# Optimization experiments

Measured on AMD Instinct MI355X. Metric: run time of the kernel, lower is better.

## Reference

```python
import jax, jax.numpy as jnp
import numpy as np

N, F_IN, H, C, E = 50000, 512, 128, 64, 800000


def setup_inputs() -> dict:
    key = jax.random.key(0)
    ks = jax.random.split(key, 20)
    stdv = 1.0 / np.sqrt(H)
    std_att = 1.0
    std_att_vec = 1.0 / np.sqrt(3.0)
    u = lambda k, shape, s: jax.random.uniform(k, shape, jnp.float32, -s, s)
    inp = {
        "x": jax.random.normal(ks[0], (N, F_IN), jnp.float32),
        "edge_row": jax.random.randint(ks[1], (E,), 0, N, jnp.int32),
        "edge_col": jax.random.randint(ks[2], (E,), 0, N, jnp.int32),
        "edge_val": jax.random.uniform(ks[3], (E,), jnp.float32) * (1.0 / 16.0),
        "weight_low": u(ks[4], (F_IN, H), stdv),
        "weight_high": u(ks[5], (F_IN, H), stdv),
        "weight_mlp": u(ks[6], (F_IN, H), stdv),
        "att_vec_low": u(ks[7], (H, 1), std_att),
        "att_vec_high": u(ks[8], (H, 1), std_att),
        "att_vec_mlp": u(ks[9], (H, 1), std_att),
        "att_vec": u(ks[10], (3, 3), std_att_vec),
        "weight_low2": u(ks[11], (H, C), stdv),
        "weight_high2": u(ks[12], (H, C), stdv),
        "weight_mlp2": u(ks[13], (H, C), stdv),
        "att_vec_low2": u(ks[14], (C, 1), std_att),
        "att_vec_high2": u(ks[15], (C, 1), std_att),
        "att_vec_mlp2": u(ks[16], (C, 1), std_att),
        "att_vec2": u(ks[17], (3, 3), std_att_vec),
    }
    return inp


def _spmm_low(row, col, val, X):
    # adj_low @ X via gather + segment-sum over edges
    return jax.ops.segment_sum(val[:, None] * X[col], row, num_segments=N)


def _attention(o_low, o_high, o_mlp, a_low, a_high, a_mlp, a_vec):
    T = 3.0
    feats = jnp.concatenate([o_low @ a_low, o_high @ a_high, o_mlp @ a_mlp], axis=1)  # [N,3]
    att = jax.nn.softmax(jax.nn.sigmoid(feats) @ a_vec / T, axis=1)
    return att[:, 0:1], att[:, 1:2], att[:, 2:3]


def _layer(X, row, col, val, W_l, W_h, W_m, a_l, a_h, a_m, a_vec):
    xl = X @ W_l
    xh = X @ W_h
    o_low = jax.nn.relu(_spmm_low(row, col, val, xl))
    o_high = jax.nn.relu(xh - _spmm_low(row, col, val, xh))  # (I - adj_low) @ xh
    o_mlp = jax.nn.relu(X @ W_m)
    al, ah, am = _attention(o_low, o_high, o_mlp, a_l, a_h, a_m, a_vec)
    return 3.0 * (al * o_low + ah * o_high + am * o_mlp)


def reference(x, edge_row, edge_col, edge_val, weight_low, weight_high, weight_mlp,
              att_vec_low, att_vec_high, att_vec_mlp, att_vec,
              weight_low2, weight_high2, weight_mlp2,
              att_vec_low2, att_vec_high2, att_vec_mlp2, att_vec2):
    h = _layer(x, edge_row, edge_col, edge_val, weight_low, weight_high, weight_mlp,
               att_vec_low, att_vec_high, att_vec_mlp, att_vec)
    out = _layer(h, edge_row, edge_col, edge_val, weight_low2, weight_high2, weight_mlp2,
                 att_vec_low2, att_vec_high2, att_vec_mlp2, att_vec2)
    return jax.nn.log_softmax(out, axis=1)
```

## Files before the change

kernel.cpp:

```cpp
#include <hip/hip_runtime.h>
#include <hip/hip_bf16.h>

#define NN 50000
#define F_IN 512
#define HH 128
#define CC 64

typedef __attribute__((ext_vector_type(8))) short short8v;
typedef __attribute__((ext_vector_type(4))) float f32x4;
typedef __attribute__((ext_vector_type(2))) float f32x2;

__device__ __forceinline__ short f2b(float f) {
    unsigned u = __builtin_bit_cast(unsigned, f);
    unsigned r = (u + 0x7fffu + ((u >> 16) & 1u)) >> 16;
    return (short)r;
}
__device__ __forceinline__ float b2f(short s) {
    unsigned u = ((unsigned)(unsigned short)s) << 16;
    return __builtin_bit_cast(float, u);
}
__device__ __forceinline__ float b2f_lo(unsigned p) {
    return __builtin_bit_cast(float, p << 16);
}
__device__ __forceinline__ float b2f_hi(unsigned p) {
    return __builtin_bit_cast(float, p & 0xffff0000u);
}

__device__ __forceinline__ f32x2 q2_lo(unsigned p) {
    return __builtin_amdgcn_cvt_pk_f32_fp8(p, false);
}
__device__ __forceinline__ f32x2 q2_hi(unsigned p) {
    return __builtin_amdgcn_cvt_pk_f32_fp8(p, true);
}

__device__ __forceinline__ int xcd_swz(int bid, int nwg) {
    int q = nwg >> 3, r = nwg & 7;
    int xcd = bid & 7, off = bid >> 3;
    return (xcd < r ? xcd * (q + 1) : r * (q + 1) + (xcd - r) * q) + off;
}

__device__ __forceinline__ void load_lds16(const short* g, short* l) {
    __builtin_amdgcn_global_load_lds(
        (const __attribute__((address_space(1))) unsigned int*)g,
        (__attribute__((address_space(3))) unsigned int*)l,
        16, 0, 0);
}

template <int K, int OUTW>
__device__ __forceinline__ void wprep_body(const float* __restrict__ W0,
                                           const float* __restrict__ W1,
                                           const float* __restrict__ W2,
                                           short* __restrict__ Bt, int id) {
    const int nth = 3 * OUTW * (K / 8);
    if (id >= nth) return;
    const int n = id / (K / 8);
    const int kq = id % (K / 8);
    const int sel = n / OUTW;
    const int c = n % OUTW;
    const float* W = sel == 0 ? W0 : (sel == 1 ? W1 : W2);
    short v[8];
#pragma unroll
    for (int j = 0; j < 8; ++j) v[j] = f2b(W[(size_t)(kq * 8 + j) * OUTW + c]);
#pragma unroll
    for (int j = 0; j < 8; ++j) Bt[(size_t)n * K + kq * 8 + j] = v[j];
}

__global__ __launch_bounds__(256) void prep0(int* __restrict__ counts, int n,
                                             const float* __restrict__ Wl,
                                             const float* __restrict__ Wh,
                                             const float* __restrict__ Wm,
                                             short* __restrict__ Bt1,
                                             const float* __restrict__ Wl2,
                                             const float* __restrict__ Wh2,
                                             const float* __restrict__ Wm2,
                                             short* __restrict__ Bt2,
                                             int nZero, int nW1) {
    const int b = blockIdx.x;
    if (b < nZero) {
        int i = b * 256 + threadIdx.x;
        if (i < n) counts[i] = 0;
    } else if (b < nZero + nW1) {
        wprep_body<F_IN, HH>(Wl, Wh, Wm, Bt1, (b - nZero) * 256 + threadIdx.x);
    } else {
        wprep_body<HH, CC>(Wl2, Wh2, Wm2, Bt2, (b - nZero - nW1) * 256 + threadIdx.x);
    }
}

__global__ __launch_bounds__(256) void hist_xconv(const int* __restrict__ erow,
                                                  int* __restrict__ counts, int E,
                                                  const float* __restrict__ x,
                                                  short* __restrict__ xb, int n8,
                                                  int nHist) {
    const int b = blockIdx.x;
    const int total = gridDim.x;
    const long hb4 = ((long)b * nHist) / total;
    const long ha4 = ((long)(b + 1) * nHist) / total;
    if (ha4 != hb4) {
        int i = (int)hb4 * 256 + threadIdx.x;
        if (i < E) atomicAdd(&counts[erow[i]], 1);
        return;
    }
    int i = (b - (int)hb4) * 256 + threadIdx.x;
    if (i >= n8) return;
    const float4* xp = (const float4*)x;
    const float4 a = xp[2 * i];
    const float4 bb = xp[2 * i + 1];
    short8v o;
    o[0] = f2b(a.x); o[1] = f2b(a.y); o[2] = f2b(a.z); o[3] = f2b(a.w);
    o[4] = f2b(bb.x); o[5] = f2b(bb.y); o[6] = f2b(bb.z); o[7] = f2b(bb.w);
    *reinterpret_cast<short8v*>(&xb[(size_t)i * 8]) = o;
}

template <int K, int BNout>
__device__ __forceinline__ void gemm_body(const short* __restrict__ A,
                                          const short* __restrict__ Bt,
                                          short* __restrict__ xl,
                                          short* __restrict__ xh,
                                          short* __restrict__ xm,
                                          int M, int wg, short* smem) {
    constexpr int BM = 128, BK = 64;
    constexpr int FM = (BNout == 128) ? 4 : 2;
    constexpr int FN = 4;
    constexpr int WM = FM * 16;
    constexpr int NKT = K / BK;
    constexpr int NBL = BNout / 32;

    short* As = smem;
    short* Bs = smem + BM * BK;

    const int tid = threadIdx.x;
    const int lane = tid & 63;
    const int wid = tid >> 6;
    const int bm = wg / 3;
    const int bn = wg % 3;
    const int m0 = bm * BM;
    const int n0 = bn * BNout;
    const int wm = (BNout == 128) ? (wid >> 1) : wid;
    const int wn = (BNout == 128) ? (wid & 1) : 0;

    const int r8 = lane >> 3;
    const int sl = (lane & 7) ^ r8;

    f32x4 acc[FM][FN];
#pragma unroll
    for (int i = 0; i < FM; ++i)
#pragma unroll
        for (int j = 0; j < FN; ++j) acc[i][j] = (f32x4){0.f, 0.f, 0.f, 0.f};

    for (int kt = 0; kt < NKT; ++kt) {
        const int k0 = kt * BK;
        __syncthreads();
#pragma unroll
        for (int i = 0; i < 4; ++i) {
            int r = (wid * 4 + i) * 8 + r8;
            int gr = m0 + r; if (gr >= M) gr = M - 1;
            load_lds16(&A[(size_t)gr * K + k0 + sl * 8], &As[(wid * 4 + i) * 512]);
        }
#pragma unroll
        for (int i = 0; i < NBL; ++i) {
            int r = (wid * NBL + i) * 8 + r8;
            load_lds16(&Bt[(size_t)(n0 + r) * K + k0 + sl * 8],
                       &Bs[(wid * NBL + i) * 512]);
        }
        __syncthreads();

        const int mrow = lane & 15;
        const int kg = lane >> 4;
#pragma unroll
        for (int kk = 0; kk < 2; ++kk) {
            short8v af[FM], bf[FN];
#pragma unroll
            for (int f = 0; f < FM; ++f) {
                int m = wm * WM + f * 16 + mrow;
                int s = kk * 4 + kg;
                af[f] = *reinterpret_cast<const short8v*>(
                    &As[m * 64 + ((s ^ (m & 7)) << 3)]);
            }
#pragma unroll
            for (int f = 0; f < FN; ++f) {
                int nr = wn * 64 + f * 16 + mrow;
                int s = kk * 4 + kg;
                bf[f] = *reinterpret_cast<const short8v*>(
                    &Bs[nr * 64 + ((s ^ (nr & 7)) << 3)]);
            }
#pragma unroll
            for (int i = 0; i < FM; ++i)
#pragma unroll
                for (int j = 0; j < FN; ++j)
                    acc[i][j] = __builtin_amdgcn_mfma_f32_16x16x32_bf16(
                        af[i], bf[j], acc[i][j], 0, 0, 0);
        }
    }

    __syncthreads();
#pragma unroll
    for (int i = 0; i < FM; ++i)
#pragma unroll
        for (int j = 0; j < FN; ++j) {
            int cc = wn * 64 + j * 16 + (lane & 15);
#pragma unroll
            for (int e = 0; e < 4; ++e) {
                int r = wm * WM + i * 16 + (lane >> 4) * 4 + e;
                smem[r * BNout + cc] = f2b(acc[i][j][e]);
            }
        }
    __syncthreads();

    short* plane = (bn == 0) ? xl : ((bn == 1) ? xh : xm);
    constexpr int CH = BM * BNout / 8;
#pragma unroll
    for (int p = 0; p < CH / 256; ++p) {
        int idx = p * 256 + tid;
        int r = idx / (BNout / 8);
        int c8 = idx % (BNout / 8);
        int grow = m0 + r;
        if (grow < M)
            *reinterpret_cast<int4*>(&plane[(size_t)grow * BNout + c8 * 8]) =
                *reinterpret_cast<const int4*>(&smem[r * BNout + c8 * 8]);
    }
}

template <int K, int BNout>
__global__ __launch_bounds__(256) void gemm_scatter(const short* __restrict__ A,
                                                    const short* __restrict__ Bt,
                                                    short* __restrict__ xl,
                                                    short* __restrict__ xh,
                                                    short* __restrict__ xm,
                                                    int M, int nGemm,
                                                    const int* __restrict__ row,
                                                    const int* __restrict__ col,
                                                    const float* __restrict__ val,
                                                    int* __restrict__ cursor,
                                                    int2* __restrict__ edges, int E,
                                                    int nScat) {
    __shared__ short smem[128 * 64 + BNout * 64];

    const int total = nGemm + nScat;
    const int swz = xcd_swz(blockIdx.x, total);
    const long ns_b = ((long)swz * nScat) / total;
    const long ns_a = ((long)(swz + 1) * nScat) / total;

    if (ns_a != ns_b) {
        int i = (int)ns_b * 256 + threadIdx.x;
        if (i < E) {
            int r = row[i];
            int p = atomicAdd(&cursor[r], 1);
            int2 rec;
            rec.x = col[i];
            rec.y = __builtin_bit_cast(int, val[i]);
            edges[p] = rec;
        }
        return;
    }
    gemm_body<K, BNout>(A, Bt, xl, xh, xm, M, swz - (int)ns_b, smem);
}

template <int K, int BNout>
__global__ __launch_bounds__(256) void gemm_mfma(const short* __restrict__ A,
                                                 const short* __restrict__ Bt,
                                                 short* __restrict__ xl,
                                                 short* __restrict__ xh,
                                                 short* __restrict__ xm,
                                                 int M) {
    __shared__ short smem[128 * 64 + BNout * 64];
    gemm_body<K, BNout>(A, Bt, xl, xh, xm, M, xcd_swz(blockIdx.x, gridDim.x), smem);
}

__global__ __launch_bounds__(256) void pack8_1(const unsigned* __restrict__ xl,
                                               const unsigned* __restrict__ xh,
                                               unsigned* __restrict__ xq, int n) {
    int i = blockIdx.x * 256 + threadIdx.x;
    if (i >= n) return;
    const unsigned vx = xl[i];
    const unsigned vh = xh[i];
    unsigned r = __builtin_amdgcn_cvt_pk_fp8_f32(b2f_lo(vx), b2f_hi(vx), 0, false);
    r = __builtin_amdgcn_cvt_pk_fp8_f32(b2f_lo(vh), b2f_hi(vh), r, true);
    xq[i] = r;
}

__global__ __launch_bounds__(256) void pack8_2(const unsigned* __restrict__ xl,
                                               const unsigned* __restrict__ xh,
                                               unsigned* __restrict__ xq, int n) {
    int i = blockIdx.x * 256 + threadIdx.x;
    if (i >= n) return;
    const unsigned vx = xl[i];
    const unsigned vh = xh[i];
    unsigned r = __builtin_amdgcn_cvt_pk_fp8_f32(b2f_lo(vx), b2f_lo(vh), 0, false);
    r = __builtin_amdgcn_cvt_pk_fp8_f32(b2f_hi(vx), b2f_hi(vh), r, true);
    xq[i] = r;
}

__global__ __launch_bounds__(256) void block_sums_kernel(const int* __restrict__ counts,
                                                         int* __restrict__ bsums, int n) {
    __shared__ int s[256];
    int tid = threadIdx.x;
    int i = blockIdx.x * 256 + tid;
    s[tid] = (i < n) ? counts[i] : 0;
    __syncthreads();
#pragma unroll
    for (int off = 128; off > 0; off >>= 1) {
        if (tid < off) s[tid] += s[tid + off];
        __syncthreads();
    }
    if (tid == 0) bsums[blockIdx.x] = s[0];
}

__global__ __launch_bounds__(256) void scan_bsums_kernel(int* __restrict__ bsums, int nb) {
    __shared__ int s[256];
    int t = threadIdx.x;
    int v = (t < nb) ? bsums[t] : 0;
    s[t] = v;
    __syncthreads();
#pragma unroll
    for (int off = 1; off < 256; off <<= 1) {
        int u = (t >= off) ? s[t - off] : 0;
        __syncthreads();
        s[t] += u;
        __syncthreads();
    }
    if (t < nb) bsums[t] = s[t] - v;
}

__global__ __launch_bounds__(256) void scan_final_kernel(const int* __restrict__ counts,
                                                         const int* __restrict__ bsums,
                                                         int* __restrict__ rowptr,
                                                         int* __restrict__ cursor, int n) {
    __shared__ int s[256];
    int tid = threadIdx.x;
    int i = blockIdx.x * 256 + tid;
    int v = (i < n) ? counts[i] : 0;
    s[tid] = v;
    __syncthreads();
#pragma unroll
    for (int off = 1; off < 256; off <<= 1) {
        int t = (tid >= off) ? s[tid - off] : 0;
        __syncthreads();
        s[tid] += t;
        __syncthreads();
    }
    int excl = s[tid] - v + bsums[blockIdx.x];
    if (i < n) {
        rowptr[i] = excl;
        cursor[i] = excl;
        if (i == n - 1) rowptr[n] = excl + v;
    }
}

__device__ __forceinline__ float wave_sum(float v) {
#pragma unroll
    for (int off = 32; off > 0; off >>= 1) v += __shfl_xor(v, off, 64);
    return v;
}
__device__ __forceinline__ float wave_max(float v) {
#pragma unroll
    for (int off = 32; off > 0; off >>= 1) v = fmaxf(v, __shfl_xor(v, off, 64));
    return v;
}

__global__ __launch_bounds__(256) void spmm_att1(const int* __restrict__ rowptr,
                                                 const int2* __restrict__ edges,
                                                 const unsigned* __restrict__ xq,
                                                 const unsigned* __restrict__ xhp,
                                                 const unsigned* __restrict__ xmp,
                                                 const float* __restrict__ a_low,
                                                 const float* __restrict__ a_high,
                                                 const float* __restrict__ a_mlp,
                                                 const float* __restrict__ av,
                                                 short* __restrict__ hb,
                                                 int n) {
    const int node = blockIdx.x * 4 + (threadIdx.x >> 6);
    const int lane = threadIdx.x & 63;
    if (node >= n) return;

    const int s = __builtin_amdgcn_readfirstlane(rowptr[node]);
    const int e = __builtin_amdgcn_readfirstlane(rowptr[node + 1]);

    float l0 = 0.f, l1 = 0.f, h0 = 0.f, h1 = 0.f;
    for (int j = s; j < e; j += 8) {
        int   cq[8];
        float vq[8];
#pragma unroll
        for (int q = 0; q < 8; ++q) {
            const int jj = min(j + q, e - 1);
            const int2 rec = edges[jj];
            cq[q] = __builtin_amdgcn_readfirstlane(rec.x);
            int vb = __builtin_amdgcn_readfirstlane(rec.y);
            float t = __builtin_bit_cast(float, vb);
            vq[q] = (j + q < e) ? t : 0.f;
        }
        unsigned p[8];
#pragma unroll
        for (int q = 0; q < 8; ++q)
            p[q] = xq[(size_t)cq[q] * 64 + lane];
#pragma unroll
        for (int q = 0; q < 8; ++q) {
            const f32x2 lo = q2_lo(p[q]);
            const f32x2 hi = q2_hi(p[q]);
            l0 += vq[q] * lo.x; l1 += vq[q] * lo.y;
            h0 += vq[q] * hi.x; h1 += vq[q] * hi.y;
        }
    }

    const unsigned xhn = xhp[(size_t)node * 64 + lane];
    const unsigned xmn = xmp[(size_t)node * 64 + lane];
    float ol0 = fmaxf(l0, 0.f);
    float ol1 = fmaxf(l1, 0.f);
    float oh0 = fmaxf(b2f_lo(xhn) - h0, 0.f);
    float oh1 = fmaxf(b2f_hi(xhn) - h1, 0.f);
    float om0 = fmaxf(b2f_lo(xmn), 0.f);
    float om1 = fmaxf(b2f_hi(xmn), 0.f);

    const float2 aL = ((const float2*)a_low)[lane];
    const float2 aH = ((const float2*)a_high)[lane];
    const float2 aM = ((const float2*)a_mlp)[lane];
    float dl = wave_sum(ol0 * aL.x + ol1 * aL.y);
    float dh = wave_sum(oh0 * aH.x + oh1 * aH.y);
    float dm = wave_sum(om0 * aM.x + om1 * aM.y);

    const float g0 = 1.f / (1.f + expf(-dl));
    const float g1 = 1.f / (1.f + expf(-dh));
    const float g2 = 1.f / (1.f + expf(-dm));
    float s0 = (g0 * av[0] + g1 * av[3] + g2 * av[6]) * (1.f / 3.f);
    float s1 = (g0 * av[1] + g1 * av[4] + g2 * av[7]) * (1.f / 3.f);
    float s2 = (g0 * av[2] + g1 * av[5] + g2 * av[8]) * (1.f / 3.f);
    float mx = fmaxf(s0, fmaxf(s1, s2));
    float e0 = expf(s0 - mx), e1 = expf(s1 - mx), e2 = expf(s2 - mx);
    float inv = 1.f / (e0 + e1 + e2);
    float at0 = e0 * inv, at1 = e1 * inv, at2 = e2 * inv;

    float ho0 = 3.f * (at0 * ol0 + at1 * oh0 + at2 * om0);
    float ho1 = 3.f * (at0 * ol1 + at1 * oh1 + at2 * om1);
    unsigned pk = (unsigned)(unsigned short)f2b(ho0) |
                  ((unsigned)(unsigned short)f2b(ho1) << 16);
    ((unsigned*)hb)[(size_t)node * 64 + lane] = pk;
}

__global__ __launch_bounds__(256) void spmm_att2(const int* __restrict__ rowptr,
                                                 const int2* __restrict__ edges,
                                                 const unsigned short* __restrict__ xq,
                                                 const short* __restrict__ xhp,
                                                 const short* __restrict__ xmp,
                                                 const float* __restrict__ a_low,
                                                 const float* __restrict__ a_high,
                                                 const float* __restrict__ a_mlp,
                                                 const float* __restrict__ av,
                                                 float* __restrict__ out,
                                                 int n) {
    const int node = blockIdx.x * 4 + (threadIdx.x >> 6);
    const int lane = threadIdx.x & 63;
    if (node >= n) return;

    const int s = __builtin_amdgcn_readfirstlane(rowptr[node]);
    const int e = __builtin_amdgcn_readfirstlane(rowptr[node + 1]);

    float accl = 0.f, acch = 0.f;
    for (int j = s; j < e; j += 8) {
        int   cq[8];
        float vq[8];
#pragma unroll
        for (int q = 0; q < 8; ++q) {
            const int jj = min(j + q, e - 1);
            const int2 rec = edges[jj];
            cq[q] = __builtin_amdgcn_readfirstlane(rec.x);
            int vb = __builtin_amdgcn_readfirstlane(rec.y);
            float t = __builtin_bit_cast(float, vb);
            vq[q] = (j + q < e) ? t : 0.f;
        }
        unsigned short p[8];
#pragma unroll
        for (int q = 0; q < 8; ++q)
            p[q] = xq[(size_t)cq[q] * 64 + lane];
#pragma unroll
        for (int q = 0; q < 8; ++q) {
            const f32x2 d = q2_lo((unsigned)p[q]);
            accl += vq[q] * d.x;
            acch += vq[q] * d.y;
        }
    }

    float ol = fmaxf(accl, 0.f);
    float oh = fmaxf(b2f(xhp[(size_t)node * 64 + lane]) - acch, 0.f);
    float om = fmaxf(b2f(xmp[(size_t)node * 64 + lane]), 0.f);

    float dl = wave_sum(ol * a_low[lane]);
    float dh = wave_sum(oh * a_high[lane]);
    float dm = wave_sum(om * a_mlp[lane]);

    const float g0 = 1.f / (1.f + expf(-dl));
    const float g1 = 1.f / (1.f + expf(-dh));
    const float g2 = 1.f / (1.f + expf(-dm));
    float s0 = (g0 * av[0] + g1 * av[3] + g2 * av[6]) * (1.f / 3.f);
    float s1 = (g0 * av[1] + g1 * av[4] + g2 * av[7]) * (1.f / 3.f);
    float s2 = (g0 * av[2] + g1 * av[5] + g2 * av[8]) * (1.f / 3.f);
    float mx3 = fmaxf(s0, fmaxf(s1, s2));
    float e0 = expf(s0 - mx3), e1 = expf(s1 - mx3), e2 = expf(s2 - mx3);
    float inv = 1.f / (e0 + e1 + e2);
    float at0 = e0 * inv, at1 = e1 * inv, at2 = e2 * inv;

    float o = 3.f * (at0 * ol + at1 * oh + at2 * om);

    float m = wave_max(o);
    float ex = expf(o - m);
    float su = wave_sum(ex);
    out[(size_t)node * 64 + lane] = o - m - logf(su);
}

extern "C" void kernel_launch(void* const* d_in, const int* in_sizes, int n_in,
                              void* d_out, int out_size, void* d_ws, size_t ws_size,
                              hipStream_t stream) {
    const float* x    = (const float*)d_in[0];
    const int*   erow = (const int*)d_in[1];
    const int*   ecol = (const int*)d_in[2];
    const float* eval = (const float*)d_in[3];
    const float* Wl   = (const float*)d_in[4];
    const float* Wh   = (const float*)d_in[5];
    const float* Wm   = (const float*)d_in[6];
    const float* al   = (const float*)d_in[7];
    const float* ah   = (const float*)d_in[8];
    const float* am   = (const float*)d_in[9];
    const float* av   = (const float*)d_in[10];
    const float* Wl2  = (const float*)d_in[11];
    const float* Wh2  = (const float*)d_in[12];
    const float* Wm2  = (const float*)d_in[13];
    const float* al2  = (const float*)d_in[14];
    const float* ah2  = (const float*)d_in[15];
    const float* am2  = (const float*)d_in[16];
    const float* av2  = (const float*)d_in[17];
    float* out = (float*)d_out;

    const int E = in_sizes[1];
    const int N = NN;

    short* ws    = (short*)d_ws;
    short* xb    = ws;
    short* xl1   = xb + (size_t)N * 512;
    short* xh1   = xl1 + (size_t)N * 128;
    short* xm1   = xh1 + (size_t)N * 128;
    short* hb    = xm1 + (size_t)N * 128;
    short* Bt1   = hb + (size_t)N * 128;
    short* Bt2   = Bt1 + 384 * 512;
    int*   ip    = (int*)(Bt2 + 192 * 128);
    int*   counts = ip;
    int*   rowptr = ip + N;
    int*   cursor = ip + 2 * N + 1;
    int*   bsums  = ip + 3 * N + 1;
    int2*  edges  = (int2*)(((size_t)(ip + 3 * N + 1 + 256) + 15) & ~(size_t)15);

    unsigned* xq1 = (unsigned*)xb;
    unsigned short* xq2 = (unsigned short*)(xb + (size_t)N * 128);

    short* xl2 = xl1;
    short* xh2 = xl1 + (size_t)N * 64;
    short* xm2 = xl1 + (size_t)N * 128;

    const int NB = (N + 255) / 256;
    const int EB = (E + 255) / 256;
    const int node_blocks = (N + 3) / 4;
    const int MT = (N + 127) / 128;
    const int XCB = (N * F_IN / 8 + 255) / 256;
    const int W1B = (3 * HH * (F_IN / 8) + 255) / 256;
    const int W2B = (3 * CC * (HH / 8) + 255) / 256;
    const int nGemm1 = MT * 3;

    prep0<<<NB + W1B + W2B, 256, 0, stream>>>(counts, N, Wl, Wh, Wm, Bt1,
                                              Wl2, Wh2, Wm2, Bt2, NB, W1B);
    hist_xconv<<<EB + XCB, 256, 0, stream>>>(erow, counts, E, x, xb,
                                             N * F_IN / 8, EB);
    block_sums_kernel<<<NB, 256, 0, stream>>>(counts, bsums, N);
    scan_bsums_kernel<<<1, 256, 0, stream>>>(bsums, NB);
    scan_final_kernel<<<NB, 256, 0, stream>>>(counts, bsums, rowptr, cursor, N);

    gemm_scatter<F_IN, HH><<<nGemm1 + EB, 256, 0, stream>>>(
        xb, Bt1, xl1, xh1, xm1, N, nGemm1, erow, ecol, eval, cursor, edges, E, EB);
    pack8_1<<<(N * 64 + 255) / 256, 256, 0, stream>>>((const unsigned*)xl1,
                                                      (const unsigned*)xh1, xq1, N * 64);
    spmm_att1<<<node_blocks, 256, 0, stream>>>(rowptr, edges, xq1,
                                               (const unsigned*)xh1,
                                               (const unsigned*)xm1,
                                               al, ah, am, av, hb, N);

    gemm_mfma<HH, CC><<<MT * 3, 256, 0, stream>>>(hb, Bt2, xl2, xh2, xm2, N);
    pack8_2<<<(N * 32 + 255) / 256, 256, 0, stream>>>((const unsigned*)xl2,
                                                      (const unsigned*)xh2,
                                                      (unsigned*)xq2, N * 32);
    spmm_att2<<<node_blocks, 256, 0, stream>>>(rowptr, edges, xq2, xh2, xm2,
                                               al2, ah2, am2, av2, out, N);
}
```

Before: 206.1 us.

## Fuse fp8 packing of low/high features into GEMM epilogue, drop pack kernels

```diff
diff --git a/kernel.cpp b/kernel.cpp
--- a/kernel.cpp
+++ b/kernel.cpp
@@ -55,8 +55,12 @@
     if (id >= nth) return;
     const int n = id / (K / 8);
     const int kq = id % (K / 8);
-    const int sel = n / OUTW;
-    const int c = n % OUTW;
+    constexpr int HB = OUTW / 2;
+    const int t = n / OUTW;
+    const int r = n % OUTW;
+    int sel, c;
+    if (t < 2) { sel = (r >= HB) ? 1 : 0; c = t * HB + (r % HB); }
+    else       { sel = 2; c = r; }
     const float* W = sel == 0 ? W0 : (sel == 1 ? W1 : W2);
     short v[8];
 #pragma unroll
@@ -114,7 +118,7 @@
 template <int K, int BNout>
 __device__ __forceinline__ void gemm_body(const short* __restrict__ A,
                                           const short* __restrict__ Bt,
-                                          short* __restrict__ xl,
+                                          unsigned* __restrict__ xq,
                                           short* __restrict__ xh,
                                           short* __restrict__ xm,
                                           int M, int wg, short* smem) {
@@ -124,6 +128,7 @@
     constexpr int WM = FM * 16;
     constexpr int NKT = K / BK;
     constexpr int NBL = BNout / 32;
+    constexpr int HB = BNout / 2;
 
     short* As = smem;
     short* Bs = smem + BM * BK;
@@ -206,24 +211,56 @@
         }
     __syncthreads();
 
-    short* plane = (bn == 0) ? xl : ((bn == 1) ? xh : xm);
-    constexpr int CH = BM * BNout / 8;
-#pragma unroll
-    for (int p = 0; p < CH / 256; ++p) {
-        int idx = p * 256 + tid;
-        int r = idx / (BNout / 8);
-        int c8 = idx % (BNout / 8);
-        int grow = m0 + r;
-        if (grow < M)
-            *reinterpret_cast<int4*>(&plane[(size_t)grow * BNout + c8 * 8]) =
-                *reinterpret_cast<const int4*>(&smem[r * BNout + c8 * 8]);
+    if (bn == 2) {
+        constexpr int CH = BM * BNout / 8;
+#pragma unroll
+        for (int p = 0; p < CH / 256; ++p) {
+            int idx = p * 256 + tid;
+            int r = idx / (BNout / 8);
+            int c8 = idx % (BNout / 8);
+            int grow = m0 + r;
+            if (grow < M)
+                *reinterpret_cast<int4*>(&xm[(size_t)grow * BNout + c8 * 8]) =
+                    *reinterpret_cast<const int4*>(&smem[r * BNout + c8 * 8]);
+        }
+    } else {
+#pragma unroll
+        for (int p = 0; p < (BM * (HB / 8)) / 256; ++p) {
+            int idx = p * 256 + tid;
+            int r = idx / (HB / 8);
+            int c8 = idx % (HB / 8);
+            int grow = m0 + r;
+            if (grow < M)
+                *reinterpret_cast<int4*>(&xh[(size_t)grow * BNout + bn * HB + c8 * 8]) =
+                    *reinterpret_cast<const int4*>(&smem[r * BNout + HB + c8 * 8]);
+        }
+#pragma unroll
+        for (int p = 0; p < (BM * (BNout / 4)) / 256; ++p) {
+            int idx = p * 256 + tid;
+            int r = idx / (BNout / 4);
+            int k = idx % (BNout / 4);
+            int grow = m0 + r;
+            if (grow < M) {
+                unsigned lw = *reinterpret_cast<const unsigned*>(&smem[r * BNout + 2 * k]);
+                unsigned hw = *reinterpret_cast<const unsigned*>(&smem[r * BNout + HB + 2 * k]);
+                unsigned w;
+                if (BNout == 128) {
+                    w = __builtin_amdgcn_cvt_pk_fp8_f32(b2f_lo(lw), b2f_hi(lw), 0, false);
+                    w = __builtin_amdgcn_cvt_pk_fp8_f32(b2f_lo(hw), b2f_hi(hw), w, true);
+                } else {
+                    w = __builtin_amdgcn_cvt_pk_fp8_f32(b2f_lo(lw), b2f_lo(hw), 0, false);
+                    w = __builtin_amdgcn_cvt_pk_fp8_f32(b2f_hi(lw), b2f_hi(hw), w, true);
+                }
+                xq[(size_t)grow * (BNout / 2) + bn * (BNout / 4) + k] = w;
+            }
+        }
     }
 }
 
 template <int K, int BNout>
 __global__ __launch_bounds__(256) void gemm_scatter(const short* __restrict__ A,
                                                     const short* __restrict__ Bt,
-                                                    short* __restrict__ xl,
+                                                    unsigned* __restrict__ xq,
                                                     short* __restrict__ xh,
                                                     short* __restrict__ xm,
                                                     int M, int nGemm,
@@ -252,42 +289,18 @@
         }
         return;
     }
-    gemm_body<K, BNout>(A, Bt, xl, xh, xm, M, swz - (int)ns_b, smem);
+    gemm_body<K, BNout>(A, Bt, xq, xh, xm, M, swz - (int)ns_b, smem);
 }
 
 template <int K, int BNout>
 __global__ __launch_bounds__(256) void gemm_mfma(const short* __restrict__ A,
                                                  const short* __restrict__ Bt,
-                                                 short* __restrict__ xl,
+                                                 unsigned* __restrict__ xq,
                                                  short* __restrict__ xh,
                                                  short* __restrict__ xm,
                                                  int M) {
     __shared__ short smem[128 * 64 + BNout * 64];
-    gemm_body<K, BNout>(A, Bt, xl, xh, xm, M, xcd_swz(blockIdx.x, gridDim.x), smem);
-}
-
-__global__ __launch_bounds__(256) void pack8_1(const unsigned* __restrict__ xl,
-                                               const unsigned* __restrict__ xh,
-                                               unsigned* __restrict__ xq, int n) {
-    int i = blockIdx.x * 256 + threadIdx.x;
-    if (i >= n) return;
-    const unsigned vx = xl[i];
-    const unsigned vh = xh[i];
-    unsigned r = __builtin_amdgcn_cvt_pk_fp8_f32(b2f_lo(vx), b2f_hi(vx), 0, false);
-    r = __builtin_amdgcn_cvt_pk_fp8_f32(b2f_lo(vh), b2f_hi(vh), r, true);
-    xq[i] = r;
-}
-
-__global__ __launch_bounds__(256) void pack8_2(const unsigned* __restrict__ xl,
-                                               const unsigned* __restrict__ xh,
-                                               unsigned* __restrict__ xq, int n) {
-    int i = blockIdx.x * 256 + threadIdx.x;
-    if (i >= n) return;
-    const unsigned vx = xl[i];
-    const unsigned vh = xh[i];
-    unsigned r = __builtin_amdgcn_cvt_pk_fp8_f32(b2f_lo(vx), b2f_lo(vh), 0, false);
-    r = __builtin_amdgcn_cvt_pk_fp8_f32(b2f_hi(vx), b2f_hi(vh), r, true);
-    xq[i] = r;
+    gemm_body<K, BNout>(A, Bt, xq, xh, xm, M, xcd_swz(blockIdx.x, gridDim.x), smem);
 }
 
 __global__ __launch_bounds__(256) void block_sums_kernel(const int* __restrict__ counts,
@@ -533,11 +546,11 @@
 
     short* ws    = (short*)d_ws;
     short* xb    = ws;
-    short* xl1   = xb + (size_t)N * 512;
-    short* xh1   = xl1 + (size_t)N * 128;
+    short* xh1   = xb + (size_t)N * 512;
     short* xm1   = xh1 + (size_t)N * 128;
     short* hb    = xm1 + (size_t)N * 128;
-    short* Bt1   = hb + (size_t)N * 128;
+    unsigned* xq1 = (unsigned*)(hb + (size_t)N * 128);
+    short* Bt1   = (short*)(xq1 + (size_t)N * 64);
     short* Bt2   = Bt1 + 384 * 512;
     int*   ip    = (int*)(Bt2 + 192 * 128);
     int*   counts = ip;
@@ -546,12 +559,9 @@
     int*   bsums  = ip + 3 * N + 1;
     int2*  edges  = (int2*)(((size_t)(ip + 3 * N + 1 + 256) + 15) & ~(size_t)15);
 
-    unsigned* xq1 = (unsigned*)xb;
-    unsigned short* xq2 = (unsigned short*)(xb + (size_t)N * 128);
-
-    short* xl2 = xl1;
-    short* xh2 = xl1 + (size_t)N * 64;
-    short* xm2 = xl1 + (size_t)N * 128;
+    unsigned* xq2 = xq1;
+    short* xh2 = xh1;
+    short* xm2 = xh1 + (size_t)N * 64;
 
     const int NB = (N + 255) / 256;
     const int EB = (E + 255) / 256;
@@ -571,18 +581,15 @@
     scan_final_kernel<<<NB, 256, 0, stream>>>(counts, bsums, rowptr, cursor, N);
 
     gemm_scatter<F_IN, HH><<<nGemm1 + EB, 256, 0, stream>>>(
-        xb, Bt1, xl1, xh1, xm1, N, nGemm1, erow, ecol, eval, cursor, edges, E, EB);
-    pack8_1<<<(N * 64 + 255) / 256, 256, 0, stream>>>((const unsigned*)xl1,
-                                                      (const unsigned*)xh1, xq1, N * 64);
+        xb, Bt1, xq1, xh1, xm1, N, nGemm1, erow, ecol, eval, cursor, edges, E, EB);
     spmm_att1<<<node_blocks, 256, 0, stream>>>(rowptr, edges, xq1,
                                                (const unsigned*)xh1,
                                                (const unsigned*)xm1,
                                                al, ah, am, av, hb, N);
 
-    gemm_mfma<HH, CC><<<MT * 3, 256, 0, stream>>>(hb, Bt2, xl2, xh2, xm2, N);
-    pack8_2<<<(N * 32 + 255) / 256, 256, 0, stream>>>((const unsigned*)xl2,
-                                                      (const unsigned*)xh2,
-                                                      (unsigned*)xq2, N * 32);
-    spmm_att2<<<node_blocks, 256, 0, stream>>>(rowptr, edges, xq2, xh2, xm2,
+    gemm_mfma<HH, CC><<<MT * 3, 256, 0, stream>>>(hb, Bt2, xq2, xh2, xm2, N);
+    spmm_att2<<<node_blocks, 256, 0, stream>>>(rowptr, edges,
+                                               (const unsigned short*)xq2,
+                                               xh2, xm2,
                                                al2, ah2, am2, av2, out, N);
 }
```

New measurement: 195.9 us. 5.0% less time.
